# Optimization experiments

Measured on AMD Instinct MI355X. Metric: run time of the kernel, lower is better.

Reference implementation:

```python
import jax, jax.numpy as jnp
import numpy as np

N = 500000      # active voxels
C_IN = 16       # input voxel feature dim
# encoder channels per stage: 32, 64, 128


def setup_inputs() -> dict:
    key = jax.random.key(0)
    ks = jax.random.split(key, 16)

    def w(k, i, o):
        return jax.random.normal(k, (i, o), dtype=jnp.float32) * (1.0 / np.sqrt(i))

    d = {}
    d['feat'] = jax.random.normal(ks[0], (N, C_IN), dtype=jnp.float32)
    d['coords'] = jax.random.randint(ks[1], (N, 4), 0, 1024, dtype=jnp.int32)
    d['W_in'] = w(ks[2], C_IN, 32)
    d['W_enc1'] = w(ks[3], 32, 32)
    d['W_enc2'] = w(ks[4], 32, 64)
    d['W_enc3'] = w(ks[5], 64, 128)
    d['W_lat1'] = w(ks[6], 32, 32)
    d['W_lat2'] = w(ks[7], 64, 64)
    d['W_lat3'] = w(ks[8], 128, 128)
    d['W_merge1'] = w(ks[9], 64, 32)    # merge: 2*C_i -> C_i
    d['W_merge2'] = w(ks[10], 128, 64)
    d['W_merge3'] = w(ks[11], 256, 128)
    d['W_up1'] = w(ks[12], 32, 32)      # upsample: C_i -> C_{i-1}
    d['W_up2'] = w(ks[13], 64, 32)
    d['W_up3'] = w(ks[14], 128, 64)
    return d


def _forward(feat, W_in, W_enc1, W_enc2, W_enc3, W_lat1, W_lat2, W_lat3,
             W_merge1, W_merge2, W_merge3, W_up1, W_up2, W_up3):
    relu = jax.nn.relu
    # conv_input + encoder (1x1 submanifold sparse convs == per-voxel matmul)
    x = relu(feat @ W_in)
    e1 = relu(x @ W_enc1)
    e2 = relu(e1 @ W_enc2)
    e3 = relu(e2 @ W_enc3)
    enc = [e1, e2, e3]
    lats = [W_lat1, W_lat2, W_lat3]
    mrgs = [W_merge1, W_merge2, W_merge3]
    ups = [W_up1, W_up2, W_up3]
    x = e3
    for i in (2, 1, 0):  # decoder stages stage_num..1
        lat = relu(enc[i] @ lats[i])                    # lateral_layer
        # cat0(x_bottom) + cat1(lat): identity-placement 1x1 convs == concat
        cat = jnp.concatenate([x, lat], axis=-1)        # [N, 2*C_i]
        merge = relu(cat @ mrgs[i])                     # merge_layer 2C->C
        red = cat.reshape(cat.shape[0], -1, 2).sum(-1)  # reduce_channel: fixed pairwise-sum conv
        x = relu((merge + red) @ ups[i])                # residual add + upsample_layer
    return x  # ret['voxel_feats']


def reference(feat, coords, W_in, W_enc1, W_enc2, W_enc3, W_lat1, W_lat2, W_lat3,
              W_merge1, W_merge2, W_merge3, W_up1, W_up2, W_up3):
    # coords define sparse structure; for 1x1 subm convs the math only touches features
    return _forward(feat, W_in, W_enc1, W_enc2, W_enc3, W_lat1, W_lat2, W_lat3,
                    W_merge1, W_merge2, W_merge3, W_up1, W_up2, W_up3)
```

## Files before the change

### kernel.cpp

```cpp
#include <hip/hip_runtime.h>

typedef unsigned short u16;
typedef _Float16 h16;
typedef __attribute__((ext_vector_type(8))) _Float16 half8;
typedef __attribute__((ext_vector_type(8))) unsigned short ushort8;
typedef __attribute__((ext_vector_type(4))) float f32x4;

#define N_STRIPS 31250
#define NPAIRS   15625
#define STRIP    16384

#define F_L0   0
#define F_L1   2
#define F_L2   4
#define F_L3   8
#define F_L4   24
#define F_L5   56
#define F_L6   120
#define F_L7   136
#define F_L8   144
#define F_L9   160
#define F_L10  164
#define F_L11  166
#define F_L12  170
#define NFRAG  172

__device__ __forceinline__ u16 hb(h16 h) { union { h16 h; u16 u; } v; v.h = h; return v.u; }

__global__ __launch_bounds__(256) void pack_w(
    const float* w0, const float* w1, const float* w2, const float* w3, const float* w4,
    const float* w5, const float* w6, const float* w7, const float* w8, const float* w9,
    const float* w10, const float* w11, const float* w12, u16* __restrict__ packed)
{
  const float* ws[13] = {w0,w1,w2,w3,w4,w5,w6,w7,w8,w9,w10,w11,w12};
  const int Ka[13]  = {16,32,32,64,128,256,128,64,128,64,32,64,32};
  const int KT[13]  = {1,1,1,2,4,8,4,2,4,2,1,2,1};
  const int CO[13]  = {32,32,64,128,128,128,64,64,64,32,32,32,32};
  const int FO[13]  = {F_L0,F_L1,F_L2,F_L3,F_L4,F_L5,F_L6,F_L7,F_L8,F_L9,F_L10,F_L11,F_L12};
  int g = blockIdx.x * 256 + threadIdx.x;
  int f = g >> 6, lane = g & 63;
  if (f >= NFRAG) return;
  int layer = 0;
#pragma unroll
  for (int i = 1; i < 13; ++i) if (f >= FO[i]) layer = i;
  int fl = f - FO[layer];
  int kt = fl % KT[layer];
  int ct = fl / KT[layer];
  int cout = CO[layer];
  int quad = lane >> 4;
  int col  = ct * 16 + (lane & 15);
  u16 thi[8], tlo[8];
#pragma unroll
  for (int j = 0; j < 8; ++j) {
    int k = kt * 32 + quad * 8 + j;
    float w = (k < Ka[layer]) ? ws[layer][k * cout + col] : 0.f;
    h16 h = (h16)w;
    h16 l = (h16)(w - (float)h);
    thi[j] = hb(h); tlo[j] = hb(l);
  }
  u16* dst = packed + ((size_t)f * 64 + lane) * 16;
  *(ushort8*)dst       = *(const ushort8*)thi;
  *(ushort8*)(dst + 8) = *(const ushort8*)tlo;
}


template<int KT>
__device__ __forceinline__ void loadA2(const h16* __restrict__ pH, int stride, int lane,
                                       half8* ah0, half8* al0, half8* ah1, half8* al1)
{
  const int base = (lane & 15) * stride + (lane >> 4) * 8;
  const int lo = 16 * stride;
#pragma unroll
  for (int kt = 0; kt < KT; ++kt) {
    ah0[kt] = *(const half8*)(pH + base + kt * 32);
    al0[kt] = *(const half8*)(pH + lo + base + kt * 32);
    ah1[kt] = *(const half8*)(pH + STRIP + base + kt * 32);
    al1[kt] = *(const half8*)(pH + STRIP + lo + base + kt * 32);
  }
}

__device__ __forceinline__ void splitw(h16* dst, int idx, int lo, float v) {
  h16 h = (h16)v;
  dst[idx]      = h;
  dst[idx + lo] = (h16)(v - (float)h);
}
__device__ __forceinline__ float red4(const h16* cat, int cs, int rr, int cc) {
  const h16* p = cat + rr * cs + 2 * cc;
  const h16* q = p + 16 * cs;
  return (float)p[0] + (float)p[1] + (float)q[0] + (float)q[1];
}

template<int KT, int CN, int EPI>
__device__ __forceinline__ void layer2(
    const half8* ah0, const half8* al0, const half8* ah1, const half8* al1,
    const h16* __restrict__ wp, int lane, int cb,
    h16* dst, int ds, int colb,
    const h16* cat, int cs,
    float* __restrict__ gout, int row0)
{
  const int l15 = lane & 15, quad = lane >> 4;
  const int dlo = 16 * ds;
#pragma unroll
  for (int ci = 0; ci < CN; ++ci) {
    const int ct = cb + ci;
    f32x4 a0 = {0.f,0.f,0.f,0.f}, a1 = {0.f,0.f,0.f,0.f};
#pragma unroll
    for (int kt = 0; kt < KT; ++kt) {
      const h16* fp = wp + (((size_t)(ct * KT + kt)) * 64 + lane) * 16;
      half8 bhv = *(const half8*)fp;
      half8 blv = *(const half8*)(fp + 8);
      a0 = __builtin_amdgcn_mfma_f32_16x16x32_f16(al0[kt], bhv, a0, 0, 0, 0);
      a0 = __builtin_amdgcn_mfma_f32_16x16x32_f16(ah0[kt], blv, a0, 0, 0, 0);
      a0 = __builtin_amdgcn_mfma_f32_16x16x32_f16(ah0[kt], bhv, a0, 0, 0, 0);
      a1 = __builtin_amdgcn_mfma_f32_16x16x32_f16(al1[kt], bhv, a1, 0, 0, 0);
      a1 = __builtin_amdgcn_mfma_f32_16x16x32_f16(ah1[kt], blv, a1, 0, 0, 0);
      a1 = __builtin_amdgcn_mfma_f32_16x16x32_f16(ah1[kt], bhv, a1, 0, 0, 0);
    }
#pragma unroll
    for (int r = 0; r < 4; ++r) {
      const int rr = quad * 4 + r;
      const int cc = ct * 16 + l15;
      float v0 = a0[r] > 0.f ? a0[r] : 0.f;
      float v1 = a1[r] > 0.f ? a1[r] : 0.f;
      if (EPI == 1) {
        v0 += red4(cat, cs, rr, cc);
        v1 += red4(cat + STRIP, cs, rr, cc);
      }
      if (EPI <= 1) {
        splitw(dst,         rr * ds + colb + cc, dlo, v0);
        splitw(dst + STRIP, rr * ds + colb + cc, dlo, v1);
      } else {
        gout[(size_t)(row0 + rr) * 32 + cc]      = v0;
        gout[(size_t)(row0 + 16 + rr) * 32 + cc] = v1;
      }
    }
  }
}

#define LAYER(KT, COT, EPI, SRC, SS, FOFF, DST, DS, COLB, CAT, CS, GOUT, ROW0)      \
  {                                                                                  \
    constexpr int CN = ((COT) >= 4) ? (COT) / 4 : 1;                                 \
    const int cb = ((COT) >= 4) ? wv * CN : wv;                                      \
    if (((COT) >= 4) || (wv < 2)) {                                                  \
      loadA2<KT>(SRC, SS, lane, ah0, al0, ah1, al1);                                 \
      layer2<KT, CN, EPI>(ah0, al0, ah1, al1, wp + (FOFF) * 1024, lane, cb,          \
                          DST, DS, COLB, CAT, CS, GOUT, ROW0);                       \
    }                                                                                \
    __syncthreads();                                                                 \
  }

__global__ __launch_bounds__(256, 2) void backbone(
    const float* __restrict__ feat, const h16* __restrict__ wp, float* __restrict__ out)
{
  __shared__ h16 lds[2 * STRIP];
  const int lane = threadIdx.x & 63;
  const int wv   = threadIdx.x >> 6;
  const int l15 = lane & 15, quad = lane >> 4;
  const int row0 = blockIdx.x * 32;

  h16* E1 = lds;            const int SE1 = 40;
  h16* E2 = lds + 1280;     const int SE2 = 72;
  h16* CT = lds + 3584;     const int SCT = 264;
  h16* MR = lds + 12032;    const int SMR = 136;

  half8 ah0[8], al0[8], ah1[8], al1[8];

  if (wv < 2) {
    h16 th0[8] = {0,0,0,0,0,0,0,0}, tl0[8] = {0,0,0,0,0,0,0,0};
    h16 th1[8] = {0,0,0,0,0,0,0,0}, tl1[8] = {0,0,0,0,0,0,0,0};
    if (quad < 2) {
      const float* s0 = feat + (size_t)(row0 + l15) * 16 + quad * 8;
      const float* s1 = feat + (size_t)(row0 + 16 + l15) * 16 + quad * 8;
#pragma unroll
      for (int j = 0; j < 8; ++j) {
        float v0 = s0[j], v1 = s1[j];
        h16 h0 = (h16)v0, h1 = (h16)v1;
        th0[j] = h0; tl0[j] = (h16)(v0 - (float)h0);
        th1[j] = h1; tl1[j] = (h16)(v1 - (float)h1);
      }
    }
    ah0[0] = *(const half8*)th0; al0[0] = *(const half8*)tl0;
    ah1[0] = *(const half8*)th1; al1[0] = *(const half8*)tl1;
    layer2<1,1,0>(ah0,al0,ah1,al1, wp + F_L0*1024, lane, wv, CT,SCT,0, nullptr,0,
                  nullptr,0);
  }
  __syncthreads();

  LAYER(1,2,0,  CT,SCT, F_L1,  E1,SE1,0,   nullptr,0, nullptr,0)
  LAYER(1,4,0,  E1,SE1, F_L2,  E2,SE2,0,   nullptr,0, nullptr,0)
  LAYER(2,8,0,  E2,SE2, F_L3,  CT,SCT,0,   nullptr,0, nullptr,0)
  LAYER(4,8,0,  CT,SCT, F_L4,  CT,SCT,128, nullptr,0, nullptr,0)
  LAYER(8,8,1,  CT,SCT, F_L5,  MR,SMR,0,   CT,SCT,   nullptr,0)
  LAYER(4,4,0,  MR,SMR, F_L6,  CT,SCT,0,   nullptr,0, nullptr,0)
  LAYER(2,4,0,  E2,SE2, F_L7,  CT,SCT,64,  nullptr,0, nullptr,0)
  LAYER(4,4,1,  CT,SCT, F_L8,  MR,SMR,0,   CT,SCT,   nullptr,0)
  LAYER(2,2,0,  MR,SMR, F_L9,  CT,SCT,0,   nullptr,0, nullptr,0)
  LAYER(1,2,0,  E1,SE1, F_L10, CT,SCT,32,  nullptr,0, nullptr,0)
  LAYER(2,2,1,  CT,SCT, F_L11, MR,SMR,0,   CT,SCT,   nullptr,0)
  LAYER(1,2,2,  MR,SMR, F_L12, nullptr,0,0, nullptr,0, out,row0)
}

extern "C" void kernel_launch(void* const* d_in, const int* in_sizes, int n_in,
                              void* d_out, int out_size, void* d_ws, size_t ws_size,
                              hipStream_t stream) {
  (void)in_sizes; (void)n_in; (void)out_size; (void)ws_size;
  u16* packed = (u16*)d_ws;

  hipLaunchKernelGGL(pack_w, dim3(43), dim3(256), 0, stream,
      (const float*)d_in[2],  (const float*)d_in[3],  (const float*)d_in[4],
      (const float*)d_in[5],  (const float*)d_in[8],  (const float*)d_in[11],
      (const float*)d_in[14], (const float*)d_in[7],  (const float*)d_in[10],
      (const float*)d_in[13], (const float*)d_in[6],  (const float*)d_in[9],
      (const float*)d_in[12], packed);

  hipLaunchKernelGGL(backbone, dim3(NPAIRS), dim3(256), 0, stream,
                     (const float*)d_in[0], (const h16*)packed, (float*)d_out);
}
```

Measured before the change: 478.4 us.

## Use 512-thread blocks, one tile per wave, with weight prefetch and concurrent layers

Doubles the block to eight waves so each wave computes a single output column tile per layer, removing the per-wave tile loop and large A-fragment register arrays. Independent lateral and decoder layers are run on different wave groups within the same barrier interval. The first weight fragment of the next layer is prefetched into registers before each barrier, and barriers use an lgkmcnt-only wait. This aims to raise wave-level parallelism and hide weight-load latency, at the cost of more idle waves in narrow layers and LDS-bound occupancy.

```diff
diff --git a/kernel.cpp b/kernel.cpp
--- a/kernel.cpp
+++ b/kernel.cpp
@@ -9,6 +9,10 @@
 #define N_STRIPS 31250
 #define NPAIRS   15625
 #define STRIP    16384
+
+#define MFMA16(A,B,C) __builtin_amdgcn_mfma_f32_16x16x32_f16(A,B,C,0,0,0)
+
+#define LBAR() asm volatile("s_waitcnt lgkmcnt(0)\n\ts_barrier" ::: "memory")
 
 #define F_L0   0
 #define F_L1   2
@@ -64,21 +68,6 @@
 }
 
 
-template<int KT>
-__device__ __forceinline__ void loadA2(const h16* __restrict__ pH, int stride, int lane,
-                                       half8* ah0, half8* al0, half8* ah1, half8* al1)
-{
-  const int base = (lane & 15) * stride + (lane >> 4) * 8;
-  const int lo = 16 * stride;
-#pragma unroll
-  for (int kt = 0; kt < KT; ++kt) {
-    ah0[kt] = *(const half8*)(pH + base + kt * 32);
-    al0[kt] = *(const half8*)(pH + lo + base + kt * 32);
-    ah1[kt] = *(const half8*)(pH + STRIP + base + kt * 32);
-    al1[kt] = *(const half8*)(pH + STRIP + lo + base + kt * 32);
-  }
-}
-
 __device__ __forceinline__ void splitw(h16* dst, int idx, int lo, float v) {
   h16 h = (h16)v;
   dst[idx]      = h;
@@ -90,66 +79,70 @@
   return (float)p[0] + (float)p[1] + (float)q[0] + (float)q[1];
 }
 
-template<int KT, int CN, int EPI>
-__device__ __forceinline__ void layer2(
-    const half8* ah0, const half8* al0, const half8* ah1, const half8* al1,
-    const h16* __restrict__ wp, int lane, int cb,
-    h16* dst, int ds, int colb,
-    const h16* cat, int cs,
+template<int EPI>
+__device__ __forceinline__ void epilogue(
+    f32x4 a0, f32x4 a1, int ct, int lane,
+    h16* dst, int ds, int colb, const h16* cat, int cs,
     float* __restrict__ gout, int row0)
 {
   const int l15 = lane & 15, quad = lane >> 4;
   const int dlo = 16 * ds;
 #pragma unroll
-  for (int ci = 0; ci < CN; ++ci) {
-    const int ct = cb + ci;
-    f32x4 a0 = {0.f,0.f,0.f,0.f}, a1 = {0.f,0.f,0.f,0.f};
-#pragma unroll
-    for (int kt = 0; kt < KT; ++kt) {
-      const h16* fp = wp + (((size_t)(ct * KT + kt)) * 64 + lane) * 16;
-      half8 bhv = *(const half8*)fp;
-      half8 blv = *(const half8*)(fp + 8);
-      a0 = __builtin_amdgcn_mfma_f32_16x16x32_f16(al0[kt], bhv, a0, 0, 0, 0);
-      a0 = __builtin_amdgcn_mfma_f32_16x16x32_f16(ah0[kt], blv, a0, 0, 0, 0);
-      a0 = __builtin_amdgcn_mfma_f32_16x16x32_f16(ah0[kt], bhv, a0, 0, 0, 0);
-      a1 = __builtin_amdgcn_mfma_f32_16x16x32_f16(al1[kt], bhv, a1, 0, 0, 0);
-      a1 = __builtin_amdgcn_mfma_f32_16x16x32_f16(ah1[kt], blv, a1, 0, 0, 0);
-      a1 = __builtin_amdgcn_mfma_f32_16x16x32_f16(ah1[kt], bhv, a1, 0, 0, 0);
-    }
-#pragma unroll
-    for (int r = 0; r < 4; ++r) {
-      const int rr = quad * 4 + r;
-      const int cc = ct * 16 + l15;
-      float v0 = a0[r] > 0.f ? a0[r] : 0.f;
-      float v1 = a1[r] > 0.f ? a1[r] : 0.f;
-      if (EPI == 1) {
-        v0 += red4(cat, cs, rr, cc);
-        v1 += red4(cat + STRIP, cs, rr, cc);
-      }
-      if (EPI <= 1) {
-        splitw(dst,         rr * ds + colb + cc, dlo, v0);
-        splitw(dst + STRIP, rr * ds + colb + cc, dlo, v1);
-      } else {
-        gout[(size_t)(row0 + rr) * 32 + cc]      = v0;
-        gout[(size_t)(row0 + 16 + rr) * 32 + cc] = v1;
-      }
-    }
-  }
-}
-
-#define LAYER(KT, COT, EPI, SRC, SS, FOFF, DST, DS, COLB, CAT, CS, GOUT, ROW0)      \
-  {                                                                                  \
-    constexpr int CN = ((COT) >= 4) ? (COT) / 4 : 1;                                 \
-    const int cb = ((COT) >= 4) ? wv * CN : wv;                                      \
-    if (((COT) >= 4) || (wv < 2)) {                                                  \
-      loadA2<KT>(SRC, SS, lane, ah0, al0, ah1, al1);                                 \
-      layer2<KT, CN, EPI>(ah0, al0, ah1, al1, wp + (FOFF) * 1024, lane, cb,          \
-                          DST, DS, COLB, CAT, CS, GOUT, ROW0);                       \
-    }                                                                                \
-    __syncthreads();                                                                 \
-  }
-
-__global__ __launch_bounds__(256, 2) void backbone(
+  for (int r = 0; r < 4; ++r) {
+    const int rr = quad * 4 + r;
+    const int cc = ct * 16 + l15;
+    float v0 = a0[r] > 0.f ? a0[r] : 0.f;
+    float v1 = a1[r] > 0.f ? a1[r] : 0.f;
+    if (EPI == 1) {
+      v0 += red4(cat, cs, rr, cc);
+      v1 += red4(cat + STRIP, cs, rr, cc);
+    }
+    if (EPI <= 1) {
+      splitw(dst,         rr * ds + colb + cc, dlo, v0);
+      splitw(dst + STRIP, rr * ds + colb + cc, dlo, v1);
+    } else {
+      gout[(size_t)(row0 + rr) * 32 + cc]      = v0;
+      gout[(size_t)(row0 + 16 + rr) * 32 + cc] = v1;
+    }
+  }
+}
+
+template<int KT, int EPI>
+__device__ __forceinline__ void layerW(
+    const h16* __restrict__ asrc, int as,
+    const h16* __restrict__ wp, int foff, int ct, int lane,
+    half8 pbh, half8 pbl,
+    h16* dst, int ds, int colb, const h16* cat, int cs,
+    float* __restrict__ gout, int row0)
+{
+  const int l15 = lane & 15, quad = lane >> 4;
+  const int abase = l15 * as + quad * 8;
+  const int alo = 16 * as;
+  f32x4 a0 = {0.f,0.f,0.f,0.f}, a1 = {0.f,0.f,0.f,0.f};
+#pragma unroll
+  for (int kt = 0; kt < KT; ++kt) {
+    half8 bhv, blv;
+    if (kt == 0) { bhv = pbh; blv = pbl; }
+    else {
+      const h16* fp = wp + (((size_t)(foff + ct * KT + kt)) * 64 + lane) * 16;
+      bhv = *(const half8*)fp;
+      blv = *(const half8*)(fp + 8);
+    }
+    half8 ah0 = *(const half8*)(asrc + abase + kt * 32);
+    half8 al0 = *(const half8*)(asrc + alo + abase + kt * 32);
+    half8 ah1 = *(const half8*)(asrc + STRIP + abase + kt * 32);
+    half8 al1 = *(const half8*)(asrc + STRIP + alo + abase + kt * 32);
+    a0 = MFMA16(al0, bhv, a0); a0 = MFMA16(ah0, blv, a0); a0 = MFMA16(ah0, bhv, a0);
+    a1 = MFMA16(al1, bhv, a1); a1 = MFMA16(ah1, blv, a1); a1 = MFMA16(ah1, bhv, a1);
+  }
+  epilogue<EPI>(a0, a1, ct, lane, dst, ds, colb, cat, cs, gout, row0);
+}
+
+#define PFB(FOFF, CT_, KT_)                                                       \
+  do { const h16* _fp = wp + (((size_t)((FOFF) + (CT_) * (KT_))) * 64 + lane) * 16; \
+       pbh = *(const half8*)_fp; pbl = *(const half8*)(_fp + 8); } while (0)
+
+__global__ __launch_bounds__(512, 4) void backbone(
     const float* __restrict__ feat, const h16* __restrict__ wp, float* __restrict__ out)
 {
   __shared__ h16 lds[2 * STRIP];
@@ -163,9 +156,10 @@
   h16* CT = lds + 3584;     const int SCT = 264;
   h16* MR = lds + 12032;    const int SMR = 136;
 
-  half8 ah0[8], al0[8], ah1[8], al1[8];
-
-  if (wv < 2) {
+  half8 pbh, pbl;
+
+  if (wv < 2) {
+    PFB(F_L0, wv, 1);
     h16 th0[8] = {0,0,0,0,0,0,0,0}, tl0[8] = {0,0,0,0,0,0,0,0};
     h16 th1[8] = {0,0,0,0,0,0,0,0}, tl1[8] = {0,0,0,0,0,0,0,0};
     if (quad < 2) {
@@ -179,25 +173,72 @@
         th1[j] = h1; tl1[j] = (h16)(v1 - (float)h1);
       }
     }
-    ah0[0] = *(const half8*)th0; al0[0] = *(const half8*)tl0;
-    ah1[0] = *(const half8*)th1; al1[0] = *(const half8*)tl1;
-    layer2<1,1,0>(ah0,al0,ah1,al1, wp + F_L0*1024, lane, wv, CT,SCT,0, nullptr,0,
-                  nullptr,0);
-  }
-  __syncthreads();
-
-  LAYER(1,2,0,  CT,SCT, F_L1,  E1,SE1,0,   nullptr,0, nullptr,0)
-  LAYER(1,4,0,  E1,SE1, F_L2,  E2,SE2,0,   nullptr,0, nullptr,0)
-  LAYER(2,8,0,  E2,SE2, F_L3,  CT,SCT,0,   nullptr,0, nullptr,0)
-  LAYER(4,8,0,  CT,SCT, F_L4,  CT,SCT,128, nullptr,0, nullptr,0)
-  LAYER(8,8,1,  CT,SCT, F_L5,  MR,SMR,0,   CT,SCT,   nullptr,0)
-  LAYER(4,4,0,  MR,SMR, F_L6,  CT,SCT,0,   nullptr,0, nullptr,0)
-  LAYER(2,4,0,  E2,SE2, F_L7,  CT,SCT,64,  nullptr,0, nullptr,0)
-  LAYER(4,4,1,  CT,SCT, F_L8,  MR,SMR,0,   CT,SCT,   nullptr,0)
-  LAYER(2,2,0,  MR,SMR, F_L9,  CT,SCT,0,   nullptr,0, nullptr,0)
-  LAYER(1,2,0,  E1,SE1, F_L10, CT,SCT,32,  nullptr,0, nullptr,0)
-  LAYER(2,2,1,  CT,SCT, F_L11, MR,SMR,0,   CT,SCT,   nullptr,0)
-  LAYER(1,2,2,  MR,SMR, F_L12, nullptr,0,0, nullptr,0, out,row0)
+    half8 ah0 = *(const half8*)th0, al0 = *(const half8*)tl0;
+    half8 ah1 = *(const half8*)th1, al1 = *(const half8*)tl1;
+    f32x4 a0 = {0.f,0.f,0.f,0.f}, a1 = {0.f,0.f,0.f,0.f};
+    a0 = MFMA16(al0, pbh, a0); a0 = MFMA16(ah0, pbl, a0); a0 = MFMA16(ah0, pbh, a0);
+    a1 = MFMA16(al1, pbh, a1); a1 = MFMA16(ah1, pbl, a1); a1 = MFMA16(ah1, pbh, a1);
+    epilogue<0>(a0, a1, wv, lane, CT, SCT, 0, nullptr, 0, nullptr, 0);
+    PFB(F_L1, wv, 1);
+  }
+  LBAR();
+
+  if (wv < 2) {
+    layerW<1,0>(CT,SCT, wp, F_L1, wv, lane, pbh,pbl, E1,SE1,0, nullptr,0, nullptr,0);
+  }
+  if (wv < 4) PFB(F_L2, wv, 1);
+  LBAR();
+
+  if (wv < 4) {
+    layerW<1,0>(E1,SE1, wp, F_L2, wv, lane, pbh,pbl, E2,SE2,0, nullptr,0, nullptr,0);
+  }
+  PFB(F_L3, wv, 2);
+  LBAR();
+
+  layerW<2,0>(E2,SE2, wp, F_L3, wv, lane, pbh,pbl, CT,SCT,0, nullptr,0, nullptr,0);
+  PFB(F_L4, wv, 4);
+  LBAR();
+
+  layerW<4,0>(CT,SCT, wp, F_L4, wv, lane, pbh,pbl, CT,SCT,128, nullptr,0, nullptr,0);
+  PFB(F_L5, wv, 8);
+  LBAR();
+
+  layerW<8,1>(CT,SCT, wp, F_L5, wv, lane, pbh,pbl, MR,SMR,0, CT,SCT, nullptr,0);
+  if (wv < 4) PFB(F_L6, wv, 4); else PFB(F_L7, wv - 4, 2);
+  LBAR();
+
+  if (wv < 4) {
+    layerW<4,0>(MR,SMR, wp, F_L6, wv, lane, pbh,pbl, CT,SCT,0,  nullptr,0, nullptr,0);
+  } else {
+    layerW<2,0>(E2,SE2, wp, F_L7, wv - 4, lane, pbh,pbl, CT,SCT,64, nullptr,0, nullptr,0);
+  }
+  if (wv < 4) PFB(F_L8, wv, 4);
+  LBAR();
+
+  if (wv < 4) {
+    layerW<4,1>(CT,SCT, wp, F_L8, wv, lane, pbh,pbl, MR,SMR,0, CT,SCT, nullptr,0);
+  }
+  if (wv < 2) PFB(F_L9, wv, 2);
+  else if (wv < 4) PFB(F_L10, wv - 2, 1);
+  LBAR();
+
+  if (wv < 2) {
+    layerW<2,0>(MR,SMR, wp, F_L9, wv, lane, pbh,pbl, CT,SCT,0,  nullptr,0, nullptr,0);
+  } else if (wv < 4) {
+    layerW<1,0>(E1,SE1, wp, F_L10, wv - 2, lane, pbh,pbl, CT,SCT,32, nullptr,0, nullptr,0);
+  }
+  if (wv < 2) PFB(F_L11, wv, 2);
+  LBAR();
+
+  if (wv < 2) {
+    layerW<2,1>(CT,SCT, wp, F_L11, wv, lane, pbh,pbl, MR,SMR,0, CT,SCT, nullptr,0);
+    PFB(F_L12, wv, 1);
+  }
+  LBAR();
+
+  if (wv < 2) {
+    layerW<1,2>(MR,SMR, wp, F_L12, wv, lane, pbh,pbl, nullptr,0,0, nullptr,0, out, row0);
+  }
 }
 
 extern "C" void kernel_launch(void* const* d_in, const int* in_sizes, int n_in,
@@ -213,6 +254,6 @@
       (const float*)d_in[13], (const float*)d_in[6],  (const float*)d_in[9],
       (const float*)d_in[12], packed);
 
-  hipLaunchKernelGGL(backbone, dim3(NPAIRS), dim3(256), 0, stream,
+  hipLaunchKernelGGL(backbone, dim3(NPAIRS), dim3(512), 0, stream,
                      (const float*)d_in[0], (const h16*)packed, (float*)d_out);
 }
```

Measured after the change: 457.5 us. 4.4% less time.
